# Optimization experiments

Measured on AMD Instinct MI355X. Metric: run time of the kernel, lower is better.

## Reference

```python
import jax, jax.numpy as jnp
import numpy as np

B, T, D = 1, 1024, 2048
F_DIM = 1408
E = 8
TOPK = 2


def setup_inputs() -> dict:
    key = jax.random.key(0)
    ks = jax.random.split(key, 5)
    x = jax.random.normal(ks[0], (B, T, D), dtype=jnp.float32)
    # torch nn.Linear weight layout: [out_features, in_features]
    gate_w = jax.random.normal(ks[1], (E, D), dtype=jnp.float32) * 0.02
    gate_proj = jax.random.normal(ks[2], (E, F_DIM, D), dtype=jnp.float32) * 0.02
    up_proj = jax.random.normal(ks[3], (E, F_DIM, D), dtype=jnp.float32) * 0.02
    down_proj = jax.random.normal(ks[4], (E, D, F_DIM), dtype=jnp.float32) * 0.02
    return {"x": x, "gate_w": gate_w, "gate_proj": gate_proj,
            "up_proj": up_proj, "down_proj": down_proj}


def reference(x, gate_w, gate_proj, up_proj, down_proj):
    b, t, d = x.shape
    x_flat = x.reshape(-1, d)                                  # [N, D]
    n = x_flat.shape[0]
    # Router: top-k logits then softmax over the selected k.
    router_logits = x_flat @ gate_w.T                          # [N, E]
    top_w, sel = jax.lax.top_k(router_logits, TOPK)            # [N, K]
    top_w = jax.nn.softmax(top_w, axis=-1)                     # [N, K]
    # Scatter routing weights into dense per-token expert weights [N, E].
    tok_ids = jnp.arange(n)[:, None]
    tw = jnp.zeros((n, E), dtype=x.dtype).at[tok_ids, sel].add(top_w)
    # Dense expert compute (mathematically identical: unselected experts get
    # zero combine weight). SwiGLU per expert.
    g = jnp.einsum('nd,efd->enf', x_flat, gate_proj)           # [E, N, F]
    u = jnp.einsum('nd,efd->enf', x_flat, up_proj)             # [E, N, F]
    h = jax.nn.silu(g) * u                                     # [E, N, F]
    eo = jnp.einsum('enf,edf->end', h, down_proj)              # [E, N, D]
    out = jnp.einsum('end,ne->nd', eo, tw)                     # [N, D]
    return out.reshape(b, t, d)
```

## Files before the change

### kernel.cpp

```cpp
#include <hip/hip_runtime.h>
#include <hip/hip_bf16.h>
#include <stdint.h>

typedef __attribute__((ext_vector_type(8))) short short8;
typedef __attribute__((ext_vector_type(4))) float f32x4;
typedef unsigned int u32;
typedef unsigned short u16;

static constexpr int N_TOK = 1024;
static constexpr int DDIM = 2048;
static constexpr int FDIM = 1408;
static constexpr int NEXP = 8;
static constexpr int MAXROWS = 3072;
static constexpr int NT128 = 24;

static constexpr size_t O_META   = 0;
static constexpr size_t O_TE128  = 256;
static constexpr size_t O_TR128  = 384;
static constexpr size_t O_ROWTOK = 768;
static constexpr size_t O_TOKROWS= O_ROWTOK + (size_t)MAXROWS * 4;
static constexpr size_t O_SEL    = O_TOKROWS + 2048 * 4;
static constexpr size_t O_W      = O_SEL + 2048 * 4;
static constexpr size_t O_XBF    = (O_W + 2048 * 4 + 255) & ~(size_t)255;
static constexpr size_t O_H      = O_XBF + (size_t)(N_TOK + 1) * DDIM * 2;
static constexpr size_t O_EO     = O_H + (size_t)MAXROWS * FDIM * 2;

static __device__ __forceinline__ u16 f2bf(float f) {
    return __builtin_bit_cast(u16, __float2bfloat16(f));
}
static __device__ __forceinline__ float bf2f(u16 s) {
    u32 u = ((u32)s) << 16;
    return __builtin_bit_cast(float, u);
}
static __device__ __forceinline__ u32 pack2(float a, float b) {
    return (u32)f2bf(a) | ((u32)f2bf(b) << 16);
}
static __device__ __forceinline__ void gload16(const void* g, void* l) {
    __builtin_amdgcn_global_load_lds(
        (const __attribute__((address_space(1))) void*)g,
        (__attribute__((address_space(3))) void*)l, 16, 0, 0);
}
#define PIN() __builtin_amdgcn_sched_barrier(0)
static __device__ __forceinline__ void sync_lgkm() {
    asm volatile("s_waitcnt lgkmcnt(0)" ::: "memory");
    __builtin_amdgcn_s_barrier();
    __builtin_amdgcn_sched_barrier(0);
}

__global__ __launch_bounds__(256) void router_kernel(
    const float* __restrict__ x, const float* __restrict__ gw,
    int* __restrict__ sel, float* __restrict__ wout, u16* __restrict__ xbf)
{
    __shared__ float xs[DDIM];
    __shared__ float lg[NEXP];
    const int tok = blockIdx.x;
    const float* xr = x + (size_t)tok * DDIM;
    for (int i = threadIdx.x; i < DDIM / 4; i += 256)
        ((float4*)xs)[i] = ((const float4*)xr)[i];
    __syncthreads();
    {
        const int i = threadIdx.x * 8;
        uint4 v;
        v.x = pack2(xs[i], xs[i + 1]);     v.y = pack2(xs[i + 2], xs[i + 3]);
        v.z = pack2(xs[i + 4], xs[i + 5]); v.w = pack2(xs[i + 6], xs[i + 7]);
        *(uint4*)(xbf + (size_t)tok * DDIM + i) = v;
        if (tok == 0)
            *(uint4*)(xbf + (size_t)N_TOK * DDIM + i) = uint4{0u, 0u, 0u, 0u};
    }
    const int wid = threadIdx.x >> 6, lane = threadIdx.x & 63;
    for (int i = 0; i < 2; i++) {
        const int e = wid * 2 + i;
        const float* g = gw + (size_t)e * DDIM;
        float s = 0.f;
        for (int k = lane; k < DDIM; k += 64) s += xs[k] * g[k];
        for (int off = 32; off > 0; off >>= 1) s += __shfl_down(s, off);
        if (lane == 0) lg[e] = s;
    }
    __syncthreads();
    if (threadIdx.x == 0) {
        int i1 = 0;
        for (int e = 1; e < NEXP; e++) if (lg[e] > lg[i1]) i1 = e;
        int i2 = -1;
        for (int e = 0; e < NEXP; e++) {
            if (e == i1) continue;
            if (i2 < 0 || lg[e] > lg[i2]) i2 = e;
        }
        const float e2 = __expf(lg[i2] - lg[i1]);
        const float w1 = 1.f / (1.f + e2);
        sel[tok * 2] = i1; sel[tok * 2 + 1] = i2;
        wout[tok * 2] = w1; wout[tok * 2 + 1] = e2 * w1;
    }
}

__global__ __launch_bounds__(512) void build_kernel(
    const int* __restrict__ sel,
    int* __restrict__ meta, int* __restrict__ te128, int* __restrict__ tr128,
    int* __restrict__ row_tok, int* __restrict__ tok_rows)
{
    __shared__ int s0[N_TOK], s1[N_TOK];
    __shared__ u16 p0[N_TOK], p1[N_TOK];
    __shared__ int counts[NEXP], offs[NEXP];
    for (int i = threadIdx.x; i < N_TOK; i += 512) {
        s0[i] = sel[i * 2]; s1[i] = sel[i * 2 + 1];
    }
    __syncthreads();
    const int e = threadIdx.x >> 6, lane = threadIdx.x & 63;
    int base = 0;
    for (int c = 0; c < N_TOK / 64; c++) {
        const int tk = c * 64 + lane;
        const int slot = (s0[tk] == e) ? 0 : ((s1[tk] == e) ? 1 : -1);
        const unsigned long long m = __ballot(slot >= 0);
        const int pre = __popcll(m & ((1ull << lane) - 1ull));
        if (slot == 0) p0[tk] = (u16)(base + pre);
        else if (slot == 1) p1[tk] = (u16)(base + pre);
        base += __popcll(m);
    }
    if (lane == 0) counts[e] = base;
    __syncthreads();
    if (threadIdx.x == 0) {
        int off = 0, n128 = 0;
        for (int qq = 0; qq < NEXP; qq++) {
            offs[qq] = off;
            const int pc = (counts[qq] + 127) & ~127;
            for (int i = 0; i < pc / 128; i++) { te128[n128] = qq; tr128[n128] = off + i * 128; n128++; }
            off += pc;
        }
        meta[0] = n128; meta[1] = off;
    }
    __syncthreads();
    const int off = offs[e];
    for (int c = 0; c < N_TOK / 64; c++) {
        const int tk = c * 64 + lane;
        const int slot = (s0[tk] == e) ? 0 : ((s1[tk] == e) ? 1 : -1);
        if (slot >= 0) {
            const int row = off + (slot ? p1[tk] : p0[tk]);
            row_tok[row] = tk;
            tok_rows[tk * 2 + slot] = row;
        }
    }
    const int cnt = counts[e];
    const int pc = (cnt + 127) & ~127;
    for (int p = cnt + lane; p < pc; p += 64) row_tok[off + p] = -1;
}

__global__ __launch_bounds__(512, 4) void mlp1_kernel(
    const u16* __restrict__ xbf,
    const float* __restrict__ gp, const float* __restrict__ upw,
    u16* __restrict__ h,
    const int* __restrict__ meta, const int* __restrict__ te128,
    const int* __restrict__ tr128, const int* __restrict__ row_tok)
{
    const int tile = blockIdx.y;
    const int nb = blockIdx.x;
    if (tile >= meta[0]) return;
    const int n0 = nb * 32;
    const int e = te128[tile];
    const int r0g = tr128[tile];

    __shared__ __align__(16) u16 As[2][128 * 64];
    __shared__ __align__(16) u16 Bs0[2][32 * 64];
    __shared__ __align__(16) u16 Bs1[2][32 * 64];

    const int t = threadIdx.x;
    const int wid = t >> 6, lane = t & 63;
    const int lr = lane & 15, lhi = lane >> 4;

    const u16* asrc[2];
    int aldsoff[2];
    #pragma unroll
    for (int j = 0; j < 2; j++) {
        const int row = wid * 16 + j * 8 + (lane >> 3);
        const int gran = (lane & 7) ^ (row & 7);
        const int tok = row_tok[r0g + row];
        asrc[j] = xbf + (size_t)(tok < 0 ? N_TOK : tok) * DDIM + gran * 8;
        aldsoff[j] = (wid * 2 + j) * 512;
    }

    const int rb = t >> 4, c4 = t & 15;
    const float* brow0 = gp  + (size_t)e * FDIM * DDIM + (size_t)(n0 + rb) * DDIM + c4 * 4;
    const float* brow1 = upw + (size_t)e * FDIM * DDIM + (size_t)(n0 + rb) * DDIM + c4 * 4;
    const int sOffB = rb * 64 + (((c4 >> 1) ^ (rb & 7)) * 8) + (c4 & 1) * 4;

    const int wm = wid * 16;

    f32x4 acc0[2], acc1[2];
    acc0[0] = acc0[1] = acc1[0] = acc1[1] = f32x4{0.f, 0.f, 0.f, 0.f};
    float4 pb0P, pb1P, pb0Q, pb1Q;

    auto STAGEA = [&](int bsel, int k0) {
        #pragma unroll
        for (int j = 0; j < 2; j++)
            gload16(asrc[j] + k0, &As[bsel][aldsoff[j]]);
    };
    auto LOADB_P = [&](int k0) {
        pb0P = *(const float4*)(brow0 + k0);
        pb1P = *(const float4*)(brow1 + k0);
    };
    auto LOADB_Q = [&](int k0) {
        pb0Q = *(const float4*)(brow0 + k0);
        pb1Q = *(const float4*)(brow1 + k0);
    };
    auto STOREB_P = [&](int bsel) {
        uint2 v0; v0.x = pack2(pb0P.x, pb0P.y); v0.y = pack2(pb0P.z, pb0P.w);
        *(uint2*)(&Bs0[bsel][sOffB]) = v0;
        uint2 v1; v1.x = pack2(pb1P.x, pb1P.y); v1.y = pack2(pb1P.z, pb1P.w);
        *(uint2*)(&Bs1[bsel][sOffB]) = v1;
    };
    auto STOREB_Q = [&](int bsel) {
        uint2 v0; v0.x = pack2(pb0Q.x, pb0Q.y); v0.y = pack2(pb0Q.z, pb0Q.w);
        *(uint2*)(&Bs0[bsel][sOffB]) = v0;
        uint2 v1; v1.x = pack2(pb1Q.x, pb1Q.y); v1.y = pack2(pb1Q.z, pb1Q.w);
        *(uint2*)(&Bs1[bsel][sOffB]) = v1;
    };
    auto COMPUTE = [&](int bsel) {
        __builtin_amdgcn_s_setprio(1);
        #pragma unroll
        for (int ks = 0; ks < 2; ks++) {
            short8 a, b0[2], b1[2];
            {
                const int rowa = wm + lr;
                const int gr = (ks * 4 + lhi) ^ (rowa & 7);
                a = *(const short8*)(&As[bsel][rowa * 64 + gr * 8]);
            }
            #pragma unroll
            for (int n = 0; n < 2; n++) {
                const int rowb = n * 16 + lr;
                const int gr = (ks * 4 + lhi) ^ (rowb & 7);
                b0[n] = *(const short8*)(&Bs0[bsel][rowb * 64 + gr * 8]);
                b1[n] = *(const short8*)(&Bs1[bsel][rowb * 64 + gr * 8]);
            }
            #pragma unroll
            for (int n = 0; n < 2; n++) {
                acc0[n] = __builtin_amdgcn_mfma_f32_16x16x32_bf16(a, b0[n], acc0[n], 0, 0, 0);
                acc1[n] = __builtin_amdgcn_mfma_f32_16x16x32_bf16(a, b1[n], acc1[n], 0, 0, 0);
            }
        }
        __builtin_amdgcn_s_setprio(0);
    };

    constexpr int NT = DDIM / 64;
    STAGEA(0, 0);
    PIN();
    LOADB_P(0);
    LOADB_Q(64);
    PIN();
    STOREB_P(0);
    sync_lgkm();
    for (int kt = 0; kt < NT; kt += 2) {
        STAGEA(1, ((kt + 1) & (NT - 1)) * 64);
        PIN();
        LOADB_P(((kt + 2) & (NT - 1)) * 64);
        PIN();
        STOREB_Q(1);
        asm volatile("s_waitcnt vmcnt(4)" ::: "memory");
        PIN();
        COMPUTE(0);
        sync_lgkm();
        STAGEA(0, ((kt + 2) & (NT - 1)) * 64);
        PIN();
        LOADB_Q(((kt + 3) & (NT - 1)) * 64);
        PIN();
        STOREB_P(0);
        asm volatile("s_waitcnt vmcnt(4)" ::: "memory");
        PIN();
        COMPUTE(1);
        sync_lgkm();
    }

    #pragma unroll
    for (int n = 0; n < 2; n++) {
        const int col = n0 + n * 16 + lr;
        #pragma unroll
        for (int j = 0; j < 4; j++) {
            const int row = r0g + wm + lhi * 4 + j;
            const float g = acc0[n][j], u = acc1[n][j];
            const float hv = g / (1.f + __expf(-g)) * u;
            h[(size_t)row * FDIM + col] = f2bf(hv);
        }
    }
}

__global__ __launch_bounds__(512, 6) void down_kernel(
    const u16* __restrict__ h, const float* __restrict__ dp,
    u16* __restrict__ eo,
    const int* __restrict__ meta, const int* __restrict__ te128,
    const int* __restrict__ tr128)
{
    const int tile = blockIdx.y;
    const int nb = blockIdx.x;
    if (tile >= meta[0]) return;
    const int n0 = nb * 64;
    const int e = te128[tile];
    const int r0g = tr128[tile];

    __shared__ __align__(16) u16 As[2][128 * 64];
    __shared__ __align__(16) u16 Bs[2][64 * 64];

    const int t = threadIdx.x;
    const int wid = t >> 6, lane = t & 63;
    const int lr = lane & 15, lhi = lane >> 4;

    const u16* asrc[2];
    int aldsoff[2];
    #pragma unroll
    for (int j = 0; j < 2; j++) {
        const int row = wid * 16 + j * 8 + (lane >> 3);
        const int gran = (lane & 7) ^ (row & 7);
        asrc[j] = h + (size_t)(r0g + row) * FDIM + gran * 8;
        aldsoff[j] = (wid * 2 + j) * 512;
    }

    const int rb = t >> 3, g8 = t & 7;
    const float* brow = dp + (size_t)e * DDIM * FDIM + (size_t)(n0 + rb) * FDIM + g8 * 8;
    const int sOffB = rb * 64 + ((g8 ^ (rb & 7)) * 8);

    const int wm = wid * 16;

    f32x4 acc[4];
    #pragma unroll
    for (int n = 0; n < 4; n++) acc[n] = f32x4{0.f,0.f,0.f,0.f};
    float4 paP, pbP, paQ, pbQ;

    auto STAGEA = [&](int bsel, int k0) {
        #pragma unroll
        for (int j = 0; j < 2; j++)
            gload16(asrc[j] + k0, &As[bsel][aldsoff[j]]);
    };
    auto LOADB_P = [&](int k0) {
        paP = *(const float4*)(brow + k0); pbP = *(const float4*)(brow + k0 + 4);
    };
    auto LOADB_Q = [&](int k0) {
        paQ = *(const float4*)(brow + k0); pbQ = *(const float4*)(brow + k0 + 4);
    };
    auto STOREB_P = [&](int bsel) {
        uint4 v; v.x = pack2(paP.x, paP.y); v.y = pack2(paP.z, paP.w);
        v.z = pack2(pbP.x, pbP.y); v.w = pack2(pbP.z, pbP.w);
        *(uint4*)(&Bs[bsel][sOffB]) = v;
    };
    auto STOREB_Q = [&](int bsel) {
        uint4 v; v.x = pack2(paQ.x, paQ.y); v.y = pack2(paQ.z, paQ.w);
        v.z = pack2(pbQ.x, pbQ.y); v.w = pack2(pbQ.z, pbQ.w);
        *(uint4*)(&Bs[bsel][sOffB]) = v;
    };
    auto COMPUTE = [&](int bsel) {
        __builtin_amdgcn_s_setprio(1);
        #pragma unroll
        for (int ks = 0; ks < 2; ks++) {
            short8 a;
            {
                const int rowa = wm + lr;
                const int gr = (ks * 4 + lhi) ^ (rowa & 7);
                a = *(const short8*)(&As[bsel][rowa * 64 + gr * 8]);
            }
            #pragma unroll
            for (int n = 0; n < 4; n++) {
                const int rowb = n * 16 + lr;
                const int gr = (ks * 4 + lhi) ^ (rowb & 7);
                const short8 b = *(const short8*)(&Bs[bsel][rowb * 64 + gr * 8]);
                acc[n] = __builtin_amdgcn_mfma_f32_16x16x32_bf16(a, b, acc[n], 0, 0, 0);
            }
        }
        __builtin_amdgcn_s_setprio(0);
    };

    constexpr int NT = FDIM / 64;
    STAGEA(0, 0);
    PIN();
    LOADB_P(0);
    LOADB_Q(64);
    PIN();
    STOREB_P(0);
    sync_lgkm();
    for (int kt = 0; kt < NT; kt += 2) {
        int k1 = kt + 1; if (k1 >= NT) k1 = 0;
        int k2 = kt + 2; if (k2 >= NT) k2 = 0;
        int k3 = kt + 3; if (k3 >= NT) k3 = 0;
        STAGEA(1, k1 * 64);
        PIN();
        LOADB_P(k2 * 64);
        PIN();
        STOREB_Q(1);
        asm volatile("s_waitcnt vmcnt(4)" ::: "memory");
        PIN();
        COMPUTE(0);
        sync_lgkm();
        STAGEA(0, k2 * 64);
        PIN();
        LOADB_Q(k3 * 64);
        PIN();
        STOREB_P(0);
        asm volatile("s_waitcnt vmcnt(4)" ::: "memory");
        PIN();
        COMPUTE(1);
        sync_lgkm();
    }

    #pragma unroll
    for (int n = 0; n < 4; n++) {
        const int col = n0 + n * 16 + lr;
        #pragma unroll
        for (int j = 0; j < 4; j++) {
            const int row = r0g + wm + lhi * 4 + j;
            eo[(size_t)row * DDIM + col] = f2bf(acc[n][j]);
        }
    }
}

__global__ __launch_bounds__(256) void combine_kernel(
    const u16* __restrict__ eo, const int* __restrict__ tok_rows,
    const float* __restrict__ w, float* __restrict__ out)
{
    const int tok = blockIdx.x;
    const int r1 = tok_rows[tok * 2], r2 = tok_rows[tok * 2 + 1];
    const float w1 = w[tok * 2], w2 = w[tok * 2 + 1];
    const int d = threadIdx.x * 8;
    const uint4 a = *(const uint4*)(eo + (size_t)r1 * DDIM + d);
    const uint4 b = *(const uint4*)(eo + (size_t)r2 * DDIM + d);
    const u32 av[4] = {a.x, a.y, a.z, a.w};
    const u32 bv[4] = {b.x, b.y, b.z, b.w};
    float4 o0, o1;
    float* op[8] = {&o0.x, &o0.y, &o0.z, &o0.w, &o1.x, &o1.y, &o1.z, &o1.w};
    #pragma unroll
    for (int i = 0; i < 4; i++) {
        *op[2 * i]     = w1 * bf2f((u16)(av[i] & 0xffff)) + w2 * bf2f((u16)(bv[i] & 0xffff));
        *op[2 * i + 1] = w1 * bf2f((u16)(av[i] >> 16))    + w2 * bf2f((u16)(bv[i] >> 16));
    }
    float4* po = (float4*)(out + (size_t)tok * DDIM + d);
    po[0] = o0; po[1] = o1;
}

extern "C" void kernel_launch(void* const* d_in, const int* in_sizes, int n_in,
                              void* d_out, int out_size, void* d_ws, size_t ws_size,
                              hipStream_t stream) {
    const float* x  = (const float*)d_in[0];
    const float* gw = (const float*)d_in[1];
    const float* gp = (const float*)d_in[2];
    const float* up = (const float*)d_in[3];
    const float* dp = (const float*)d_in[4];
    float* out = (float*)d_out;
    char* ws = (char*)d_ws;

    int*   meta     = (int*)(ws + O_META);
    int*   te128    = (int*)(ws + O_TE128);
    int*   tr128    = (int*)(ws + O_TR128);
    int*   row_tok  = (int*)(ws + O_ROWTOK);
    int*   tok_rows = (int*)(ws + O_TOKROWS);
    int*   sel      = (int*)(ws + O_SEL);
    float* w        = (float*)(ws + O_W);
    u16*   xbf      = (u16*)(ws + O_XBF);
    u16*   h        = (u16*)(ws + O_H);
    u16*   eo       = (u16*)(ws + O_EO);

    router_kernel<<<N_TOK, 256, 0, stream>>>(x, gw, sel, w, xbf);
    build_kernel<<<1, 512, 0, stream>>>(sel, meta, te128, tr128, row_tok, tok_rows);
    mlp1_kernel<<<dim3(FDIM / 32, NT128), 512, 0, stream>>>(
        xbf, gp, up, h, meta, te128, tr128, row_tok);
    down_kernel<<<dim3(DDIM / 64, NT128), 512, 0, stream>>>(
        h, dp, eo, meta, te128, tr128);
    combine_kernel<<<N_TOK, 256, 0, stream>>>(eo, tok_rows, w, out);
}
```

Before: 178.5 us.

## Load activation fragments directly into registers instead of staging through LDS

```diff
diff --git a/kernel.cpp b/kernel.cpp
--- a/kernel.cpp
+++ b/kernel.cpp
@@ -34,11 +34,6 @@
 }
 static __device__ __forceinline__ u32 pack2(float a, float b) {
     return (u32)f2bf(a) | ((u32)f2bf(b) << 16);
-}
-static __device__ __forceinline__ void gload16(const void* g, void* l) {
-    __builtin_amdgcn_global_load_lds(
-        (const __attribute__((address_space(1))) void*)g,
-        (__attribute__((address_space(3))) void*)l, 16, 0, 0);
 }
 #define PIN() __builtin_amdgcn_sched_barrier(0)
 static __device__ __forceinline__ void sync_lgkm() {
@@ -143,7 +138,7 @@
     for (int p = cnt + lane; p < pc; p += 64) row_tok[off + p] = -1;
 }
 
-__global__ __launch_bounds__(512, 4) void mlp1_kernel(
+__global__ __launch_bounds__(512, 6) void mlp1_kernel(
     const u16* __restrict__ xbf,
     const float* __restrict__ gp, const float* __restrict__ upw,
     u16* __restrict__ h,
@@ -157,40 +152,34 @@
     const int e = te128[tile];
     const int r0g = tr128[tile];
 
-    __shared__ __align__(16) u16 As[2][128 * 64];
     __shared__ __align__(16) u16 Bs0[2][32 * 64];
     __shared__ __align__(16) u16 Bs1[2][32 * 64];
 
     const int t = threadIdx.x;
     const int wid = t >> 6, lane = t & 63;
     const int lr = lane & 15, lhi = lane >> 4;
-
-    const u16* asrc[2];
-    int aldsoff[2];
-    #pragma unroll
-    for (int j = 0; j < 2; j++) {
-        const int row = wid * 16 + j * 8 + (lane >> 3);
-        const int gran = (lane & 7) ^ (row & 7);
-        const int tok = row_tok[r0g + row];
-        asrc[j] = xbf + (size_t)(tok < 0 ? N_TOK : tok) * DDIM + gran * 8;
-        aldsoff[j] = (wid * 2 + j) * 512;
-    }
+    const int wm = wid * 16;
+
+    const int tokA = row_tok[r0g + wm + lr];
+    const u16* aptr = xbf + (size_t)(tokA < 0 ? N_TOK : tokA) * DDIM + lhi * 8;
 
     const int rb = t >> 4, c4 = t & 15;
     const float* brow0 = gp  + (size_t)e * FDIM * DDIM + (size_t)(n0 + rb) * DDIM + c4 * 4;
     const float* brow1 = upw + (size_t)e * FDIM * DDIM + (size_t)(n0 + rb) * DDIM + c4 * 4;
     const int sOffB = rb * 64 + (((c4 >> 1) ^ (rb & 7)) * 8) + (c4 & 1) * 4;
 
-    const int wm = wid * 16;
-
     f32x4 acc0[2], acc1[2];
     acc0[0] = acc0[1] = acc1[0] = acc1[1] = f32x4{0.f, 0.f, 0.f, 0.f};
+    short8 aP0, aP1, aQ0, aQ1;
     float4 pb0P, pb1P, pb0Q, pb1Q;
 
-    auto STAGEA = [&](int bsel, int k0) {
-        #pragma unroll
-        for (int j = 0; j < 2; j++)
-            gload16(asrc[j] + k0, &As[bsel][aldsoff[j]]);
+    auto LOADA_P = [&](int k0) {
+        aP0 = *(const short8*)(aptr + k0);
+        aP1 = *(const short8*)(aptr + k0 + 32);
+    };
+    auto LOADA_Q = [&](int k0) {
+        aQ0 = *(const short8*)(aptr + k0);
+        aQ1 = *(const short8*)(aptr + k0 + 32);
     };
     auto LOADB_P = [&](int k0) {
         pb0P = *(const float4*)(brow0 + k0);
@@ -212,16 +201,12 @@
         uint2 v1; v1.x = pack2(pb1Q.x, pb1Q.y); v1.y = pack2(pb1Q.z, pb1Q.w);
         *(uint2*)(&Bs1[bsel][sOffB]) = v1;
     };
-    auto COMPUTE = [&](int bsel) {
+    auto COMPUTE = [&](int bsel, const short8& a0, const short8& a1) {
         __builtin_amdgcn_s_setprio(1);
         #pragma unroll
         for (int ks = 0; ks < 2; ks++) {
-            short8 a, b0[2], b1[2];
-            {
-                const int rowa = wm + lr;
-                const int gr = (ks * 4 + lhi) ^ (rowa & 7);
-                a = *(const short8*)(&As[bsel][rowa * 64 + gr * 8]);
-            }
+            const short8 a = ks ? a1 : a0;
+            short8 b0[2], b1[2];
             #pragma unroll
             for (int n = 0; n < 2; n++) {
                 const int rowb = n * 16 + lr;
@@ -239,31 +224,35 @@
     };
 
     constexpr int NT = DDIM / 64;
-    STAGEA(0, 0);
-    PIN();
     LOADB_P(0);
+    LOADA_P(0);
     LOADB_Q(64);
+    LOADA_Q(64);
     PIN();
     STOREB_P(0);
+    PIN();
+    LOADB_P(2 * 64);
     sync_lgkm();
     for (int kt = 0; kt < NT; kt += 2) {
-        STAGEA(1, ((kt + 1) & (NT - 1)) * 64);
-        PIN();
-        LOADB_P(((kt + 2) & (NT - 1)) * 64);
-        PIN();
         STOREB_Q(1);
-        asm volatile("s_waitcnt vmcnt(4)" ::: "memory");
-        PIN();
-        COMPUTE(0);
+        PIN();
+        LOADB_Q(((kt + 3) & (NT - 1)) * 64);
+        PIN();
+        asm volatile("s_waitcnt vmcnt(6)" ::: "memory");
+        PIN();
+        COMPUTE(0, aP0, aP1);
+        LOADA_P(((kt + 2) & (NT - 1)) * 64);
+        PIN();
         sync_lgkm();
-        STAGEA(0, ((kt + 2) & (NT - 1)) * 64);
-        PIN();
-        LOADB_Q(((kt + 3) & (NT - 1)) * 64);
-        PIN();
         STOREB_P(0);
-        asm volatile("s_waitcnt vmcnt(4)" ::: "memory");
-        PIN();
-        COMPUTE(1);
+        PIN();
+        LOADB_P(((kt + 4) & (NT - 1)) * 64);
+        PIN();
+        asm volatile("s_waitcnt vmcnt(6)" ::: "memory");
+        PIN();
+        COMPUTE(1, aQ0, aQ1);
+        LOADA_Q(((kt + 3) & (NT - 1)) * 64);
+        PIN();
         sync_lgkm();
     }
 
@@ -293,38 +282,32 @@
     const int e = te128[tile];
     const int r0g = tr128[tile];
 
-    __shared__ __align__(16) u16 As[2][128 * 64];
     __shared__ __align__(16) u16 Bs[2][64 * 64];
 
     const int t = threadIdx.x;
     const int wid = t >> 6, lane = t & 63;
     const int lr = lane & 15, lhi = lane >> 4;
-
-    const u16* asrc[2];
-    int aldsoff[2];
-    #pragma unroll
-    for (int j = 0; j < 2; j++) {
-        const int row = wid * 16 + j * 8 + (lane >> 3);
-        const int gran = (lane & 7) ^ (row & 7);
-        asrc[j] = h + (size_t)(r0g + row) * FDIM + gran * 8;
-        aldsoff[j] = (wid * 2 + j) * 512;
-    }
+    const int wm = wid * 16;
+
+    const u16* aptr = h + (size_t)(r0g + wm + lr) * FDIM + lhi * 8;
 
     const int rb = t >> 3, g8 = t & 7;
     const float* brow = dp + (size_t)e * DDIM * FDIM + (size_t)(n0 + rb) * FDIM + g8 * 8;
     const int sOffB = rb * 64 + ((g8 ^ (rb & 7)) * 8);
 
-    const int wm = wid * 16;
-
     f32x4 acc[4];
     #pragma unroll
     for (int n = 0; n < 4; n++) acc[n] = f32x4{0.f,0.f,0.f,0.f};
+    short8 aP0, aP1, aQ0, aQ1;
     float4 paP, pbP, paQ, pbQ;
 
-    auto STAGEA = [&](int bsel, int k0) {
-        #pragma unroll
-        for (int j = 0; j < 2; j++)
-            gload16(asrc[j] + k0, &As[bsel][aldsoff[j]]);
+    auto LOADA_P = [&](int k0) {
+        aP0 = *(const short8*)(aptr + k0);
+        aP1 = *(const short8*)(aptr + k0 + 32);
+    };
+    auto LOADA_Q = [&](int k0) {
+        aQ0 = *(const short8*)(aptr + k0);
+        aQ1 = *(const short8*)(aptr + k0 + 32);
     };
     auto LOADB_P = [&](int k0) {
         paP = *(const float4*)(brow + k0); pbP = *(const float4*)(brow + k0 + 4);
@@ -342,16 +325,11 @@
         v.z = pack2(pbQ.x, pbQ.y); v.w = pack2(pbQ.z, pbQ.w);
         *(uint4*)(&Bs[bsel][sOffB]) = v;
     };
-    auto COMPUTE = [&](int bsel) {
+    auto COMPUTE = [&](int bsel, const short8& a0, const short8& a1) {
         __builtin_amdgcn_s_setprio(1);
         #pragma unroll
         for (int ks = 0; ks < 2; ks++) {
-            short8 a;
-            {
-                const int rowa = wm + lr;
-                const int gr = (ks * 4 + lhi) ^ (rowa & 7);
-                a = *(const short8*)(&As[bsel][rowa * 64 + gr * 8]);
-            }
+            const short8 a = ks ? a1 : a0;
             #pragma unroll
             for (int n = 0; n < 4; n++) {
                 const int rowb = n * 16 + lr;
@@ -364,34 +342,38 @@
     };
 
     constexpr int NT = FDIM / 64;
-    STAGEA(0, 0);
-    PIN();
     LOADB_P(0);
+    LOADA_P(0);
     LOADB_Q(64);
+    LOADA_Q(64);
     PIN();
     STOREB_P(0);
+    PIN();
+    LOADB_P(2 * 64);
     sync_lgkm();
     for (int kt = 0; kt < NT; kt += 2) {
-        int k1 = kt + 1; if (k1 >= NT) k1 = 0;
         int k2 = kt + 2; if (k2 >= NT) k2 = 0;
         int k3 = kt + 3; if (k3 >= NT) k3 = 0;
-        STAGEA(1, k1 * 64);
-        PIN();
-        LOADB_P(k2 * 64);
-        PIN();
+        int k4 = kt + 4; if (k4 >= NT) k4 = 0;
         STOREB_Q(1);
-        asm volatile("s_waitcnt vmcnt(4)" ::: "memory");
-        PIN();
-        COMPUTE(0);
+        PIN();
+        LOADB_Q(k3 * 64);
+        PIN();
+        asm volatile("s_waitcnt vmcnt(6)" ::: "memory");
+        PIN();
+        COMPUTE(0, aP0, aP1);
+        LOADA_P(k2 * 64);
+        PIN();
         sync_lgkm();
-        STAGEA(0, k2 * 64);
-        PIN();
-        LOADB_Q(k3 * 64);
-        PIN();
         STOREB_P(0);
-        asm volatile("s_waitcnt vmcnt(4)" ::: "memory");
-        PIN();
-        COMPUTE(1);
+        PIN();
+        LOADB_P(k4 * 64);
+        PIN();
+        asm volatile("s_waitcnt vmcnt(6)" ::: "memory");
+        PIN();
+        COMPUTE(1, aQ0, aQ1);
+        LOADA_Q(k3 * 64);
+        PIN();
         sync_lgkm();
     }
 
```

Measured after the change: 192.0 us. +7.5%, slower.

## Use 256-row expert tiles with 1024-thread blocks in both GEMM kernels

Applied to the files above, without the earlier changes.

```diff
diff --git a/kernel.cpp b/kernel.cpp
--- a/kernel.cpp
+++ b/kernel.cpp
@@ -11,12 +11,12 @@
 static constexpr int DDIM = 2048;
 static constexpr int FDIM = 1408;
 static constexpr int NEXP = 8;
-static constexpr int MAXROWS = 3072;
-static constexpr int NT128 = 24;
+static constexpr int MAXROWS = 4096;
+static constexpr int NT256 = 16;
 
 static constexpr size_t O_META   = 0;
-static constexpr size_t O_TE128  = 256;
-static constexpr size_t O_TR128  = 384;
+static constexpr size_t O_TE     = 256;
+static constexpr size_t O_TR     = 384;
 static constexpr size_t O_ROWTOK = 768;
 static constexpr size_t O_TOKROWS= O_ROWTOK + (size_t)MAXROWS * 4;
 static constexpr size_t O_SEL    = O_TOKROWS + 2048 * 4;
@@ -94,7 +94,7 @@
 
 __global__ __launch_bounds__(512) void build_kernel(
     const int* __restrict__ sel,
-    int* __restrict__ meta, int* __restrict__ te128, int* __restrict__ tr128,
+    int* __restrict__ meta, int* __restrict__ te, int* __restrict__ tr,
     int* __restrict__ row_tok, int* __restrict__ tok_rows)
 {
     __shared__ int s0[N_TOK], s1[N_TOK];
@@ -118,14 +118,14 @@
     if (lane == 0) counts[e] = base;
     __syncthreads();
     if (threadIdx.x == 0) {
-        int off = 0, n128 = 0;
+        int off = 0, nt = 0;
         for (int qq = 0; qq < NEXP; qq++) {
             offs[qq] = off;
-            const int pc = (counts[qq] + 127) & ~127;
-            for (int i = 0; i < pc / 128; i++) { te128[n128] = qq; tr128[n128] = off + i * 128; n128++; }
+            const int pc = (counts[qq] + 255) & ~255;
+            for (int i = 0; i < pc / 256; i++) { te[nt] = qq; tr[nt] = off + i * 256; nt++; }
             off += pc;
         }
-        meta[0] = n128; meta[1] = off;
+        meta[0] = nt; meta[1] = off;
     }
     __syncthreads();
     const int off = offs[e];
@@ -139,78 +139,68 @@
         }
     }
     const int cnt = counts[e];
-    const int pc = (cnt + 127) & ~127;
+    const int pc = (cnt + 255) & ~255;
     for (int p = cnt + lane; p < pc; p += 64) row_tok[off + p] = -1;
 }
 
-__global__ __launch_bounds__(512, 4) void mlp1_kernel(
+__global__ __launch_bounds__(1024, 8) void mlp1_kernel(
     const u16* __restrict__ xbf,
     const float* __restrict__ gp, const float* __restrict__ upw,
     u16* __restrict__ h,
-    const int* __restrict__ meta, const int* __restrict__ te128,
-    const int* __restrict__ tr128, const int* __restrict__ row_tok)
+    const int* __restrict__ meta, const int* __restrict__ te,
+    const int* __restrict__ tr, const int* __restrict__ row_tok)
 {
     const int tile = blockIdx.y;
     const int nb = blockIdx.x;
     if (tile >= meta[0]) return;
     const int n0 = nb * 32;
-    const int e = te128[tile];
-    const int r0g = tr128[tile];
-
-    __shared__ __align__(16) u16 As[2][128 * 64];
-    __shared__ __align__(16) u16 Bs0[2][32 * 64];
-    __shared__ __align__(16) u16 Bs1[2][32 * 64];
+    const int e = te[tile];
+    const int r0g = tr[tile];
+
+    __shared__ __align__(16) u16 As[2][256 * 64];
+    __shared__ __align__(16) u16 Bs[2][2][32 * 64];
 
     const int t = threadIdx.x;
     const int wid = t >> 6, lane = t & 63;
     const int lr = lane & 15, lhi = lane >> 4;
+    const int wm = wid * 16;
 
     const u16* asrc[2];
     int aldsoff[2];
     #pragma unroll
     for (int j = 0; j < 2; j++) {
-        const int row = wid * 16 + j * 8 + (lane >> 3);
+        const int row = wm + j * 8 + (lane >> 3);
         const int gran = (lane & 7) ^ (row & 7);
         const int tok = row_tok[r0g + row];
         asrc[j] = xbf + (size_t)(tok < 0 ? N_TOK : tok) * DDIM + gran * 8;
         aldsoff[j] = (wid * 2 + j) * 512;
     }
 
-    const int rb = t >> 4, c4 = t & 15;
-    const float* brow0 = gp  + (size_t)e * FDIM * DDIM + (size_t)(n0 + rb) * DDIM + c4 * 4;
-    const float* brow1 = upw + (size_t)e * FDIM * DDIM + (size_t)(n0 + rb) * DDIM + c4 * 4;
+    const int mat = t >> 9, tl = t & 511;
+    const int rb = tl >> 4, c4 = tl & 15;
+    const float* brow = (mat ? upw : gp)
+        + (size_t)e * FDIM * DDIM + (size_t)(n0 + rb) * DDIM + c4 * 4;
+    u16* bst = &Bs[mat][0][0];
     const int sOffB = rb * 64 + (((c4 >> 1) ^ (rb & 7)) * 8) + (c4 & 1) * 4;
-
-    const int wm = wid * 16;
 
     f32x4 acc0[2], acc1[2];
     acc0[0] = acc0[1] = acc1[0] = acc1[1] = f32x4{0.f, 0.f, 0.f, 0.f};
-    float4 pb0P, pb1P, pb0Q, pb1Q;
+    float4 pbP, pbQ;
 
     auto STAGEA = [&](int bsel, int k0) {
         #pragma unroll
         for (int j = 0; j < 2; j++)
             gload16(asrc[j] + k0, &As[bsel][aldsoff[j]]);
     };
-    auto LOADB_P = [&](int k0) {
-        pb0P = *(const float4*)(brow0 + k0);
-        pb1P = *(const float4*)(brow1 + k0);
-    };
-    auto LOADB_Q = [&](int k0) {
-        pb0Q = *(const float4*)(brow0 + k0);
-        pb1Q = *(const float4*)(brow1 + k0);
-    };
+    auto LOADB_P = [&](int k0) { pbP = *(const float4*)(brow + k0); };
+    auto LOADB_Q = [&](int k0) { pbQ = *(const float4*)(brow + k0); };
     auto STOREB_P = [&](int bsel) {
-        uint2 v0; v0.x = pack2(pb0P.x, pb0P.y); v0.y = pack2(pb0P.z, pb0P.w);
-        *(uint2*)(&Bs0[bsel][sOffB]) = v0;
-        uint2 v1; v1.x = pack2(pb1P.x, pb1P.y); v1.y = pack2(pb1P.z, pb1P.w);
-        *(uint2*)(&Bs1[bsel][sOffB]) = v1;
+        uint2 v; v.x = pack2(pbP.x, pbP.y); v.y = pack2(pbP.z, pbP.w);
+        *(uint2*)(bst + bsel * 2048 + sOffB) = v;
     };
     auto STOREB_Q = [&](int bsel) {
-        uint2 v0; v0.x = pack2(pb0Q.x, pb0Q.y); v0.y = pack2(pb0Q.z, pb0Q.w);
-        *(uint2*)(&Bs0[bsel][sOffB]) = v0;
-        uint2 v1; v1.x = pack2(pb1Q.x, pb1Q.y); v1.y = pack2(pb1Q.z, pb1Q.w);
-        *(uint2*)(&Bs1[bsel][sOffB]) = v1;
+        uint2 v; v.x = pack2(pbQ.x, pbQ.y); v.y = pack2(pbQ.z, pbQ.w);
+        *(uint2*)(bst + bsel * 2048 + sOffB) = v;
     };
     auto COMPUTE = [&](int bsel) {
         __builtin_amdgcn_s_setprio(1);
@@ -226,8 +216,8 @@
             for (int n = 0; n < 2; n++) {
                 const int rowb = n * 16 + lr;
                 const int gr = (ks * 4 + lhi) ^ (rowb & 7);
-                b0[n] = *(const short8*)(&Bs0[bsel][rowb * 64 + gr * 8]);
-                b1[n] = *(const short8*)(&Bs1[bsel][rowb * 64 + gr * 8]);
+                b0[n] = *(const short8*)(&Bs[0][bsel][rowb * 64 + gr * 8]);
+                b1[n] = *(const short8*)(&Bs[1][bsel][rowb * 64 + gr * 8]);
             }
             #pragma unroll
             for (int n = 0; n < 2; n++) {
@@ -252,7 +242,7 @@
         LOADB_P(((kt + 2) & (NT - 1)) * 64);
         PIN();
         STOREB_Q(1);
-        asm volatile("s_waitcnt vmcnt(4)" ::: "memory");
+        asm volatile("s_waitcnt vmcnt(3)" ::: "memory");
         PIN();
         COMPUTE(0);
         sync_lgkm();
@@ -261,7 +251,7 @@
         LOADB_Q(((kt + 3) & (NT - 1)) * 64);
         PIN();
         STOREB_P(0);
-        asm volatile("s_waitcnt vmcnt(4)" ::: "memory");
+        asm volatile("s_waitcnt vmcnt(3)" ::: "memory");
         PIN();
         COMPUTE(1);
         sync_lgkm();
@@ -280,67 +270,60 @@
     }
 }
 
-__global__ __launch_bounds__(512, 6) void down_kernel(
+__global__ __launch_bounds__(1024, 8) void down_kernel(
     const u16* __restrict__ h, const float* __restrict__ dp,
     u16* __restrict__ eo,
-    const int* __restrict__ meta, const int* __restrict__ te128,
-    const int* __restrict__ tr128)
+    const int* __restrict__ meta, const int* __restrict__ te,
+    const int* __restrict__ tr)
 {
     const int tile = blockIdx.y;
     const int nb = blockIdx.x;
     if (tile >= meta[0]) return;
     const int n0 = nb * 64;
-    const int e = te128[tile];
-    const int r0g = tr128[tile];
-
-    __shared__ __align__(16) u16 As[2][128 * 64];
+    const int e = te[tile];
+    const int r0g = tr[tile];
+
+    __shared__ __align__(16) u16 As[2][256 * 64];
     __shared__ __align__(16) u16 Bs[2][64 * 64];
 
     const int t = threadIdx.x;
     const int wid = t >> 6, lane = t & 63;
     const int lr = lane & 15, lhi = lane >> 4;
+    const int wm = wid * 16;
 
     const u16* asrc[2];
     int aldsoff[2];
     #pragma unroll
     for (int j = 0; j < 2; j++) {
-        const int row = wid * 16 + j * 8 + (lane >> 3);
+        const int row = wm + j * 8 + (lane >> 3);
         const int gran = (lane & 7) ^ (row & 7);
         asrc[j] = h + (size_t)(r0g + row) * FDIM + gran * 8;
         aldsoff[j] = (wid * 2 + j) * 512;
     }
 
-    const int rb = t >> 3, g8 = t & 7;
-    const float* brow = dp + (size_t)e * DDIM * FDIM + (size_t)(n0 + rb) * FDIM + g8 * 8;
-    const int sOffB = rb * 64 + ((g8 ^ (rb & 7)) * 8);
-
-    const int wm = wid * 16;
+    const int rb = t >> 4, c4 = t & 15;
+    const float* brow = dp + (size_t)e * DDIM * FDIM + (size_t)(n0 + rb) * FDIM + c4 * 4;
+    const int sOffB = rb * 64 + (((c4 >> 1) ^ (rb & 7)) * 8) + (c4 & 1) * 4;
 
     f32x4 acc[4];
     #pragma unroll
     for (int n = 0; n < 4; n++) acc[n] = f32x4{0.f,0.f,0.f,0.f};
-    float4 paP, pbP, paQ, pbQ;
+    float4 pbP, pbQ;
 
     auto STAGEA = [&](int bsel, int k0) {
         #pragma unroll
         for (int j = 0; j < 2; j++)
             gload16(asrc[j] + k0, &As[bsel][aldsoff[j]]);
     };
-    auto LOADB_P = [&](int k0) {
-        paP = *(const float4*)(brow + k0); pbP = *(const float4*)(brow + k0 + 4);
-    };
-    auto LOADB_Q = [&](int k0) {
-        paQ = *(const float4*)(brow + k0); pbQ = *(const float4*)(brow + k0 + 4);
-    };
+    auto LOADB_P = [&](int k0) { pbP = *(const float4*)(brow + k0); };
+    auto LOADB_Q = [&](int k0) { pbQ = *(const float4*)(brow + k0); };
     auto STOREB_P = [&](int bsel) {
-        uint4 v; v.x = pack2(paP.x, paP.y); v.y = pack2(paP.z, paP.w);
-        v.z = pack2(pbP.x, pbP.y); v.w = pack2(pbP.z, pbP.w);
-        *(uint4*)(&Bs[bsel][sOffB]) = v;
+        uint2 v; v.x = pack2(pbP.x, pbP.y); v.y = pack2(pbP.z, pbP.w);
+        *(uint2*)(&Bs[bsel][sOffB]) = v;
     };
     auto STOREB_Q = [&](int bsel) {
-        uint4 v; v.x = pack2(paQ.x, paQ.y); v.y = pack2(paQ.z, paQ.w);
-        v.z = pack2(pbQ.x, pbQ.y); v.w = pack2(pbQ.z, pbQ.w);
-        *(uint4*)(&Bs[bsel][sOffB]) = v;
+        uint2 v; v.x = pack2(pbQ.x, pbQ.y); v.y = pack2(pbQ.z, pbQ.w);
+        *(uint2*)(&Bs[bsel][sOffB]) = v;
     };
     auto COMPUTE = [&](int bsel) {
         __builtin_amdgcn_s_setprio(1);
@@ -380,7 +363,7 @@
         LOADB_P(k2 * 64);
         PIN();
         STOREB_Q(1);
-        asm volatile("s_waitcnt vmcnt(4)" ::: "memory");
+        asm volatile("s_waitcnt vmcnt(3)" ::: "memory");
         PIN();
         COMPUTE(0);
         sync_lgkm();
@@ -389,7 +372,7 @@
         LOADB_Q(k3 * 64);
         PIN();
         STOREB_P(0);
-        asm volatile("s_waitcnt vmcnt(4)" ::: "memory");
+        asm volatile("s_waitcnt vmcnt(3)" ::: "memory");
         PIN();
         COMPUTE(1);
         sync_lgkm();
@@ -441,8 +424,8 @@
     char* ws = (char*)d_ws;
 
     int*   meta     = (int*)(ws + O_META);
-    int*   te128    = (int*)(ws + O_TE128);
-    int*   tr128    = (int*)(ws + O_TR128);
+    int*   te       = (int*)(ws + O_TE);
+    int*   tr       = (int*)(ws + O_TR);
     int*   row_tok  = (int*)(ws + O_ROWTOK);
     int*   tok_rows = (int*)(ws + O_TOKROWS);
     int*   sel      = (int*)(ws + O_SEL);
@@ -452,10 +435,10 @@
     u16*   eo       = (u16*)(ws + O_EO);
 
     router_kernel<<<N_TOK, 256, 0, stream>>>(x, gw, sel, w, xbf);
-    build_kernel<<<1, 512, 0, stream>>>(sel, meta, te128, tr128, row_tok, tok_rows);
-    mlp1_kernel<<<dim3(FDIM / 32, NT128), 512, 0, stream>>>(
-        xbf, gp, up, h, meta, te128, tr128, row_tok);
-    down_kernel<<<dim3(DDIM / 64, NT128), 512, 0, stream>>>(
-        h, dp, eo, meta, te128, tr128);
+    build_kernel<<<1, 512, 0, stream>>>(sel, meta, te, tr, row_tok, tok_rows);
+    mlp1_kernel<<<dim3(FDIM / 32, NT256), 1024, 0, stream>>>(
+        xbf, gp, up, h, meta, te, tr, row_tok);
+    down_kernel<<<dim3(DDIM / 64, NT256), 1024, 0, stream>>>(
+        h, dp, eo, meta, te, tr);
     combine_kernel<<<N_TOK, 256, 0, stream>>>(eo, tok_rows, w, out);
 }
```

After: 174.7 us (median of 3 runs). 1.02x faster.

## Use 256-row tiles with 1024-thread blocks in down-projection kernel

Applied to the files above, without the earlier changes.

```diff
diff --git a/kernel.cpp b/kernel.cpp
--- a/kernel.cpp
+++ b/kernel.cpp
@@ -11,12 +11,15 @@
 static constexpr int DDIM = 2048;
 static constexpr int FDIM = 1408;
 static constexpr int NEXP = 8;
-static constexpr int MAXROWS = 3072;
+static constexpr int MAXROWS = 4096;
 static constexpr int NT128 = 24;
+static constexpr int NT256 = 16;
 
 static constexpr size_t O_META   = 0;
 static constexpr size_t O_TE128  = 256;
 static constexpr size_t O_TR128  = 384;
+static constexpr size_t O_TE256  = 512;
+static constexpr size_t O_TR256  = 640;
 static constexpr size_t O_ROWTOK = 768;
 static constexpr size_t O_TOKROWS= O_ROWTOK + (size_t)MAXROWS * 4;
 static constexpr size_t O_SEL    = O_TOKROWS + 2048 * 4;
@@ -95,6 +98,7 @@
 __global__ __launch_bounds__(512) void build_kernel(
     const int* __restrict__ sel,
     int* __restrict__ meta, int* __restrict__ te128, int* __restrict__ tr128,
+    int* __restrict__ te256, int* __restrict__ tr256,
     int* __restrict__ row_tok, int* __restrict__ tok_rows)
 {
     __shared__ int s0[N_TOK], s1[N_TOK];
@@ -118,14 +122,16 @@
     if (lane == 0) counts[e] = base;
     __syncthreads();
     if (threadIdx.x == 0) {
-        int off = 0, n128 = 0;
+        int off = 0, n128 = 0, n256 = 0;
         for (int qq = 0; qq < NEXP; qq++) {
             offs[qq] = off;
-            const int pc = (counts[qq] + 127) & ~127;
-            for (int i = 0; i < pc / 128; i++) { te128[n128] = qq; tr128[n128] = off + i * 128; n128++; }
+            const int cnt = counts[qq];
+            const int pc = (cnt + 255) & ~255;
+            for (int i = 0; i * 128 < cnt; i++) { te128[n128] = qq; tr128[n128] = off + i * 128; n128++; }
+            for (int i = 0; i < pc / 256; i++)  { te256[n256] = qq; tr256[n256] = off + i * 256; n256++; }
             off += pc;
         }
-        meta[0] = n128; meta[1] = off;
+        meta[0] = n128; meta[1] = off; meta[2] = n256;
     }
     __syncthreads();
     const int off = offs[e];
@@ -139,7 +145,7 @@
         }
     }
     const int cnt = counts[e];
-    const int pc = (cnt + 127) & ~127;
+    const int pc = (cnt + 255) & ~255;
     for (int p = cnt + lane; p < pc; p += 64) row_tok[off + p] = -1;
 }
 
@@ -164,12 +170,13 @@
     const int t = threadIdx.x;
     const int wid = t >> 6, lane = t & 63;
     const int lr = lane & 15, lhi = lane >> 4;
+    const int wm = wid * 16;
 
     const u16* asrc[2];
     int aldsoff[2];
     #pragma unroll
     for (int j = 0; j < 2; j++) {
-        const int row = wid * 16 + j * 8 + (lane >> 3);
+        const int row = wm + j * 8 + (lane >> 3);
         const int gran = (lane & 7) ^ (row & 7);
         const int tok = row_tok[r0g + row];
         asrc[j] = xbf + (size_t)(tok < 0 ? N_TOK : tok) * DDIM + gran * 8;
@@ -180,8 +187,6 @@
     const float* brow0 = gp  + (size_t)e * FDIM * DDIM + (size_t)(n0 + rb) * DDIM + c4 * 4;
     const float* brow1 = upw + (size_t)e * FDIM * DDIM + (size_t)(n0 + rb) * DDIM + c4 * 4;
     const int sOffB = rb * 64 + (((c4 >> 1) ^ (rb & 7)) * 8) + (c4 & 1) * 4;
-
-    const int wm = wid * 16;
 
     f32x4 acc0[2], acc1[2];
     acc0[0] = acc0[1] = acc1[0] = acc1[1] = f32x4{0.f, 0.f, 0.f, 0.f};
@@ -280,67 +285,60 @@
     }
 }
 
-__global__ __launch_bounds__(512, 6) void down_kernel(
+__global__ __launch_bounds__(1024, 8) void down_kernel(
     const u16* __restrict__ h, const float* __restrict__ dp,
     u16* __restrict__ eo,
-    const int* __restrict__ meta, const int* __restrict__ te128,
-    const int* __restrict__ tr128)
+    const int* __restrict__ meta, const int* __restrict__ te256,
+    const int* __restrict__ tr256)
 {
     const int tile = blockIdx.y;
     const int nb = blockIdx.x;
-    if (tile >= meta[0]) return;
+    if (tile >= meta[2]) return;
     const int n0 = nb * 64;
-    const int e = te128[tile];
-    const int r0g = tr128[tile];
-
-    __shared__ __align__(16) u16 As[2][128 * 64];
+    const int e = te256[tile];
+    const int r0g = tr256[tile];
+
+    __shared__ __align__(16) u16 As[2][256 * 64];
     __shared__ __align__(16) u16 Bs[2][64 * 64];
 
     const int t = threadIdx.x;
     const int wid = t >> 6, lane = t & 63;
     const int lr = lane & 15, lhi = lane >> 4;
+    const int wm = wid * 16;
 
     const u16* asrc[2];
     int aldsoff[2];
     #pragma unroll
     for (int j = 0; j < 2; j++) {
-        const int row = wid * 16 + j * 8 + (lane >> 3);
+        const int row = wm + j * 8 + (lane >> 3);
         const int gran = (lane & 7) ^ (row & 7);
         asrc[j] = h + (size_t)(r0g + row) * FDIM + gran * 8;
         aldsoff[j] = (wid * 2 + j) * 512;
     }
 
-    const int rb = t >> 3, g8 = t & 7;
-    const float* brow = dp + (size_t)e * DDIM * FDIM + (size_t)(n0 + rb) * FDIM + g8 * 8;
-    const int sOffB = rb * 64 + ((g8 ^ (rb & 7)) * 8);
-
-    const int wm = wid * 16;
+    const int rb = t >> 4, c4 = t & 15;
+    const float* brow = dp + (size_t)e * DDIM * FDIM + (size_t)(n0 + rb) * FDIM + c4 * 4;
+    const int sOffB = rb * 64 + (((c4 >> 1) ^ (rb & 7)) * 8) + (c4 & 1) * 4;
 
     f32x4 acc[4];
     #pragma unroll
     for (int n = 0; n < 4; n++) acc[n] = f32x4{0.f,0.f,0.f,0.f};
-    float4 paP, pbP, paQ, pbQ;
+    float4 pbP, pbQ;
 
     auto STAGEA = [&](int bsel, int k0) {
         #pragma unroll
         for (int j = 0; j < 2; j++)
             gload16(asrc[j] + k0, &As[bsel][aldsoff[j]]);
     };
-    auto LOADB_P = [&](int k0) {
-        paP = *(const float4*)(brow + k0); pbP = *(const float4*)(brow + k0 + 4);
-    };
-    auto LOADB_Q = [&](int k0) {
-        paQ = *(const float4*)(brow + k0); pbQ = *(const float4*)(brow + k0 + 4);
-    };
+    auto LOADB_P = [&](int k0) { pbP = *(const float4*)(brow + k0); };
+    auto LOADB_Q = [&](int k0) { pbQ = *(const float4*)(brow + k0); };
     auto STOREB_P = [&](int bsel) {
-        uint4 v; v.x = pack2(paP.x, paP.y); v.y = pack2(paP.z, paP.w);
-        v.z = pack2(pbP.x, pbP.y); v.w = pack2(pbP.z, pbP.w);
-        *(uint4*)(&Bs[bsel][sOffB]) = v;
+        uint2 v; v.x = pack2(pbP.x, pbP.y); v.y = pack2(pbP.z, pbP.w);
+        *(uint2*)(&Bs[bsel][sOffB]) = v;
     };
     auto STOREB_Q = [&](int bsel) {
-        uint4 v; v.x = pack2(paQ.x, paQ.y); v.y = pack2(paQ.z, paQ.w);
-        v.z = pack2(pbQ.x, pbQ.y); v.w = pack2(pbQ.z, pbQ.w);
-        *(uint4*)(&Bs[bsel][sOffB]) = v;
+        uint2 v; v.x = pack2(pbQ.x, pbQ.y); v.y = pack2(pbQ.z, pbQ.w);
+        *(uint2*)(&Bs[bsel][sOffB]) = v;
     };
     auto COMPUTE = [&](int bsel) {
         __builtin_amdgcn_s_setprio(1);
@@ -380,7 +378,7 @@
         LOADB_P(k2 * 64);
         PIN();
         STOREB_Q(1);
-        asm volatile("s_waitcnt vmcnt(4)" ::: "memory");
+        asm volatile("s_waitcnt vmcnt(3)" ::: "memory");
         PIN();
         COMPUTE(0);
         sync_lgkm();
@@ -389,7 +387,7 @@
         LOADB_Q(k3 * 64);
         PIN();
         STOREB_P(0);
-        asm volatile("s_waitcnt vmcnt(4)" ::: "memory");
+        asm volatile("s_waitcnt vmcnt(3)" ::: "memory");
         PIN();
         COMPUTE(1);
         sync_lgkm();
@@ -443,6 +441,8 @@
     int*   meta     = (int*)(ws + O_META);
     int*   te128    = (int*)(ws + O_TE128);
     int*   tr128    = (int*)(ws + O_TR128);
+    int*   te256    = (int*)(ws + O_TE256);
+    int*   tr256    = (int*)(ws + O_TR256);
     int*   row_tok  = (int*)(ws + O_ROWTOK);
     int*   tok_rows = (int*)(ws + O_TOKROWS);
     int*   sel      = (int*)(ws + O_SEL);
@@ -452,10 +452,11 @@
     u16*   eo       = (u16*)(ws + O_EO);
 
     router_kernel<<<N_TOK, 256, 0, stream>>>(x, gw, sel, w, xbf);
-    build_kernel<<<1, 512, 0, stream>>>(sel, meta, te128, tr128, row_tok, tok_rows);
+    build_kernel<<<1, 512, 0, stream>>>(sel, meta, te128, tr128, te256, tr256,
+                                        row_tok, tok_rows);
     mlp1_kernel<<<dim3(FDIM / 32, NT128), 512, 0, stream>>>(
         xbf, gp, up, h, meta, te128, tr128, row_tok);
-    down_kernel<<<dim3(DDIM / 64, NT128), 512, 0, stream>>>(
-        h, dp, eo, meta, te128, tr128);
+    down_kernel<<<dim3(DDIM / 64, NT256), 1024, 0, stream>>>(
+        h, dp, eo, meta, te256, tr256);
     combine_kernel<<<N_TOK, 256, 0, stream>>>(eo, tok_rows, w, out);
 }
```

After: 183.1 us. 1.03x slower.
